# Kernel tuning notes

Measured on AMD Instinct MI355X. Metric: run time of the kernel, lower is better.

## Reference

```python
import jax, jax.numpy as jnp
import numpy as np

PAIRS = [(0,1),(1,2),(2,3),(0,4),(4,5),(5,6),(0,7),(7,8),(8,9),(9,10),(8,11),(11,12),(12,13),(8,14),(14,15),(15,16)]
END_JOINTS = np.array([3, 6, 10, 13, 16])  # leaf joints gated in the trailing loop
N, DIM, HID, B = 17, 512, 384, 8192
LN_EPS = 1e-5


def _build_adj():
    A = np.zeros((N, N), np.float32)
    for p, c in PAIRS:
        A[p, c] = A[c, p] = 1.0
    A += np.eye(N, dtype=np.float32)
    dinv = 1.0 / np.sqrt(A.sum(1))
    return jnp.asarray(dinv[:, None] * A * dinv[None, :])


def setup_inputs() -> dict:
    key = jax.random.key(0)
    ks = jax.random.split(key, 8)
    return {
        "x_gcn": jax.random.normal(ks[0], (B, N, DIM), jnp.float32),
        "bone_features": jax.random.normal(ks[1], (B, N, 192), jnp.float32),
        "adj": _build_adj(),
        "g1": jnp.ones((DIM,), jnp.float32),
        "b1": jnp.zeros((DIM,), jnp.float32),
        "W1": jax.random.normal(ks[2], (2, DIM, HID), jnp.float32) * 0.02,
        "M1": jax.random.uniform(ks[3], (N, HID), jnp.float32),
        "A2_1": jnp.ones((N, N), jnp.float32),
        "bias1": jnp.zeros((HID,), jnp.float32),
        "W2": jax.random.normal(ks[4], (2, HID, DIM), jnp.float32) * 0.02,
        "M2": jax.random.uniform(ks[5], (N, DIM), jnp.float32),
        "A2_2": jnp.ones((N, N), jnp.float32),
        "bias2": jnp.zeros((DIM,), jnp.float32),
        "g2": jnp.ones((DIM,), jnp.float32),
        "b2": jnp.zeros((DIM,), jnp.float32),
    }


def _ln(x, g, b):
    m = x.mean(-1, keepdims=True)
    v = jnp.mean((x - m) ** 2, axis=-1, keepdims=True)
    return (x - m) * jax.lax.rsqrt(v + LN_EPS) * g + b


def _mgc(x, W, M, adj_base, A2, bias):
    # Modulated graph conv: separate self / neighbor transforms, per-node modulation M.
    h0 = jnp.einsum('bnc,cd->bnd', x, W[0])
    h1 = jnp.einsum('bnc,cd->bnd', x, W[1])
    adj = adj_base + A2
    adj = (adj.T + adj) * 0.5
    E = jnp.eye(N, dtype=x.dtype)
    out = jnp.einsum('vw,bwd->bvd', adj * E, M * h0) + jnp.einsum('vw,bwd->bvd', adj * (1.0 - E), M * h1)
    return out + bias


def reference(x_gcn, bone_features, adj, g1, b1, W1, M1, A2_1, bias1,
              W2, M2, A2_2, bias2, g2, b2):
    h = _ln(x_gcn, g1, b1)
    h = _mgc(h, W1, M1, adj, A2_1, bias1)
    h = jax.nn.gelu(h, approximate=False)  # torch nn.GELU default = exact erf
    h = _mgc(h, W2, M2, adj, A2_2, bias2)
    h = _ln(h, g2, b2)
    xp = x_gcn + h  # drop_path=0 -> identity

    # bone gating: first chunk(3, -1) slice, mean over channels, sigmoid gate
    c = bone_features.shape[-1]
    bone_chunk = bone_features[..., : -(-c // 3)]  # torch.chunk first piece (ceil)
    gate = jax.nn.sigmoid(bone_chunk.mean(-1, keepdims=True) * 0.01)  # (B, N, 1)
    mask = jnp.zeros((N,), xp.dtype).at[jnp.asarray(END_JOINTS)].set(1.0)
    return xp * (1.0 + 0.03 * gate * mask[None, :, None])
```

## Files before the change

### kernel.cpp

```cpp
#include <hip/hip_runtime.h>
#include <hip/hip_bf16.h>

typedef __attribute__((ext_vector_type(8))) short s16x8;
typedef __attribute__((ext_vector_type(4))) float f32x4;

typedef __attribute__((address_space(1))) void v_as1;
typedef __attribute__((address_space(3))) void v_as3;

__device__ __forceinline__ void gload16(const void* g, void* l) {
    __builtin_amdgcn_global_load_lds((const v_as1*)g, (v_as3*)l, 16, 0, 0);
}

__device__ __forceinline__ unsigned short f2bf(float f) {
    unsigned u = __float_as_uint(f);
    unsigned r = (u + 0x7FFFu + ((u >> 16) & 1u)) >> 16;
    return (unsigned short)r;
}
__device__ __forceinline__ float frombf(unsigned short u) {
    return __uint_as_float(((unsigned)u) << 16);
}

__global__ void prep_w1(const float* __restrict__ W1, unsigned short* __restrict__ w1t) {
    int idx = blockIdx.x * 256 + threadIdx.x;
    if (idx >= 768 * 512) return;
    int n = idx >> 9, k = idx & 511;
    int g = (n >= 384) ? 1 : 0;
    int d = n - g * 384;
    w1t[idx] = f2bf(W1[((long)g * 512 + k) * 384 + d]);
}

__global__ void prep_w2(const float* __restrict__ W2, unsigned short* __restrict__ w2t) {
    int idx = blockIdx.x * 256 + threadIdx.x;
    if (idx >= 1024 * 384) return;
    int n = idx / 384, k = idx % 384;
    int g = (n >= 512) ? 1 : 0;
    int d = n - g * 512;
    w2t[idx] = f2bf(W2[((long)g * 384 + k) * 512 + d]);
}

__global__ void prep_adj(const float* __restrict__ adj, const float* __restrict__ A2a,
                         const float* __restrict__ A2b, float* __restrict__ coef1,
                         float* __restrict__ coef2) {
    int t = threadIdx.x;
    if (t < 289) {
        int v = t / 17, w = t % 17;
        int tt = w * 17 + v;
        float s1 = 0.5f * (adj[t] + A2a[t] + adj[tt] + A2a[tt]);
        float s2 = 0.5f * (adj[t] + A2b[t] + adj[tt] + A2b[tt]);
        coef1[t] = (v == w) ? 0.f : s1;
        coef2[t] = (v == w) ? 0.f : s2;
        if (v == w) { coef1[289 + v] = s1; coef2[289 + v] = s2; }
    }
}

__global__ __launch_bounds__(256) void ln1_kernel(const float* __restrict__ x,
                                                  const float* __restrict__ g,
                                                  const float* __restrict__ b,
                                                  unsigned short* __restrict__ y, int rows) {
    int wave = threadIdx.x >> 6, lane = threadIdx.x & 63;
    long row = (long)blockIdx.x * 4 + wave;
    if (row >= rows) return;
    const float4* xr = (const float4*)(x + row * 512);
    float4 v0 = xr[lane];
    float4 v1 = xr[lane + 64];
    float s = v0.x + v0.y + v0.z + v0.w + v1.x + v1.y + v1.z + v1.w;
    float q = v0.x * v0.x + v0.y * v0.y + v0.z * v0.z + v0.w * v0.w +
              v1.x * v1.x + v1.y * v1.y + v1.z * v1.z + v1.w * v1.w;
    #pragma unroll
    for (int off = 32; off; off >>= 1) { s += __shfl_xor(s, off); q += __shfl_xor(q, off); }
    float mean = s * (1.f / 512.f);
    float var  = q * (1.f / 512.f) - mean * mean;
    float rstd = rsqrtf(var + 1e-5f);
    const float4* gr = (const float4*)g;
    const float4* br = (const float4*)b;
    ushort4* yr = (ushort4*)(y + row * 512);
    #pragma unroll
    for (int i = 0; i < 2; ++i) {
        float4 vv = i ? v1 : v0;
        float4 gg = gr[lane + 64 * i];
        float4 bb = br[lane + 64 * i];
        ushort4 o;
        o.x = f2bf((vv.x - mean) * rstd * gg.x + bb.x);
        o.y = f2bf((vv.y - mean) * rstd * gg.y + bb.y);
        o.z = f2bf((vv.z - mean) * rstd * gg.z + bb.z);
        o.w = f2bf((vv.w - mean) * rstd * gg.w + bb.w);
        yr[lane + 64 * i] = o;
    }
}

__global__ __launch_bounds__(256) void gemm_bt_kernel(const unsigned short* __restrict__ A,
                                                      const unsigned short* __restrict__ Bt,
                                                      unsigned short* __restrict__ C,
                                                      int K, int Ncols, int NBX) {
    __shared__ __align__(16) unsigned short As[128 * 64];
    __shared__ __align__(16) unsigned short Bs[128 * 64];
    const int t = threadIdx.x;
    const int lane = t & 63;
    const int w = t >> 6;
    const int wr = w >> 1, wc = w & 1;

    const int nwg = gridDim.x;
    const int q = nwg >> 3, r = nwg & 7;
    const int xcd = blockIdx.x & 7, pos = blockIdx.x >> 3;
    const int wgid = (xcd < r ? xcd * (q + 1) : r * (q + 1) + (xcd - r) * q) + pos;
    const int bx = wgid % NBX;
    const int by = wgid / NBX;
    const long row0 = (long)by * 128;
    const long col0 = (long)bx * 128;

    const int lm = lane & 15;
    const int g4 = lane >> 4;
    const int swz0 = ((g4 ^ (lm & 7)) * 8);
    const int swz1 = (((g4 + 4) ^ (lm & 7)) * 8);

    f32x4 acc[4][4];
    #pragma unroll
    for (int m = 0; m < 4; ++m)
        #pragma unroll
        for (int n = 0; n < 4; ++n) acc[m][n] = (f32x4)0.f;

    const int srow = t >> 3;
    const int sslot = (t & 7) ^ (srow & 7);
    const unsigned short* aBase = A + (row0 + srow) * K + sslot * 8;
    const unsigned short* bBase = Bt + (col0 + srow) * K + sslot * 8;
    unsigned short* aDst = &As[w * 512];
    unsigned short* bDst = &Bs[w * 512];

    const int ktiles = K >> 6;
    for (int kt = 0; kt < ktiles; ++kt) {
        const long ko = (long)kt * 64;
        __syncthreads();
        #pragma unroll
        for (int rr = 0; rr < 4; ++rr) {
            gload16(aBase + (long)(rr * 32) * K + ko, aDst + rr * 2048);
            gload16(bBase + (long)(rr * 32) * K + ko, bDst + rr * 2048);
        }
        __syncthreads();
        #pragma unroll
        for (int kk = 0; kk < 2; ++kk) {
            const int so = kk ? swz1 : swz0;
            s16x8 af[4], bfv[4];
            #pragma unroll
            for (int m = 0; m < 4; ++m)
                af[m] = *(const s16x8*)&As[(wr * 64 + m * 16 + lm) * 64 + so];
            #pragma unroll
            for (int n = 0; n < 4; ++n)
                bfv[n] = *(const s16x8*)&Bs[(wc * 64 + n * 16 + lm) * 64 + so];
            #pragma unroll
            for (int m = 0; m < 4; ++m)
                #pragma unroll
                for (int n = 0; n < 4; ++n)
                    acc[m][n] = __builtin_amdgcn_mfma_f32_16x16x32_bf16(af[m], bfv[n], acc[m][n], 0, 0, 0);
        }
    }
    const int r4 = (lane >> 4) * 4;
    #pragma unroll
    for (int m = 0; m < 4; ++m) {
        #pragma unroll
        for (int j = 0; j < 4; ++j) {
            long grow = row0 + wr * 64 + m * 16 + r4 + j;
            unsigned short* crow = C + grow * Ncols + col0 + wc * 64 + lm;
            #pragma unroll
            for (int n = 0; n < 4; ++n) crow[n * 16] = f2bf(acc[m][n][j]);
        }
    }
}

__global__ __launch_bounds__(384) void mixgelu_kernel(const unsigned short* __restrict__ h,
                                                      const float* __restrict__ M1,
                                                      const float* __restrict__ coef,
                                                      const float* __restrict__ bias,
                                                      unsigned short* __restrict__ z) {
    const int t = threadIdx.x;
    const int half = t / 192;
    const int tt = t - half * 192;
    const int d0 = tt * 2;
    const long b = blockIdx.x * 2 + half;
    const unsigned short* hb = h + b * 17 * 768;

    float ax[17], ay[17];
    const float bx = bias[d0], by = bias[d0 + 1];
    #pragma unroll
    for (int v = 0; v < 17; ++v) {
        float dg = coef[289 + v];
        float2 m = *(const float2*)(M1 + v * 384 + d0);
        ushort2 hv = *(const ushort2*)(hb + v * 768 + d0);
        ax[v] = dg * m.x * frombf(hv.x) + bx;
        ay[v] = dg * m.y * frombf(hv.y) + by;
    }
    #pragma unroll
    for (int w = 0; w < 17; ++w) {
        float2 m = *(const float2*)(M1 + w * 384 + d0);
        ushort2 hw = *(const ushort2*)(hb + w * 768 + 384 + d0);
        float px = m.x * frombf(hw.x);
        float py = m.y * frombf(hw.y);
        #pragma unroll
        for (int v = 0; v < 17; ++v) {
            float c = coef[v * 17 + w];
            ax[v] += c * px;
            ay[v] += c * py;
        }
    }
    unsigned short* zb = z + b * 17 * 384 + d0;
    #pragma unroll
    for (int v = 0; v < 17; ++v) {
        float gx = 0.5f * ax[v] * (1.f + erff(ax[v] * 0.70710678118f));
        float gy = 0.5f * ay[v] * (1.f + erff(ay[v] * 0.70710678118f));
        ushort2 o; o.x = f2bf(gx); o.y = f2bf(gy);
        *(ushort2*)(zb + v * 384) = o;
    }
}

__global__ __launch_bounds__(256) void final_kernel(const unsigned short* __restrict__ h2,
                                                    const float* __restrict__ x,
                                                    const float* __restrict__ bone,
                                                    const float* __restrict__ M2,
                                                    const float* __restrict__ coef,
                                                    const float* __restrict__ bias2,
                                                    const float* __restrict__ g2,
                                                    const float* __restrict__ b2,
                                                    float* __restrict__ out) {
    __shared__ float gate[17];
    __shared__ float red[17][8];
    const int t = threadIdx.x, lane = t & 63, wave = t >> 6;
    const int d0 = t * 2;
    const long b = blockIdx.x;

    #pragma unroll
    for (int v0 = 0; v0 < 20; v0 += 4) {
        int v = v0 + wave;
        if (v < 17) {
            float s = bone[(b * 17 + v) * 192 + lane];
            #pragma unroll
            for (int off = 32; off; off >>= 1) s += __shfl_xor(s, off);
            if (lane == 0) gate[v] = 1.f / (1.f + expf(-s * (0.01f / 64.f)));
        }
    }

    const unsigned short* hb = h2 + b * 17 * 1024;
    float ax[17], ay[17];
    const float bx = bias2[d0], by = bias2[d0 + 1];
    #pragma unroll
    for (int v = 0; v < 17; ++v) {
        float dg = coef[289 + v];
        float2 m = *(const float2*)(M2 + v * 512 + d0);
        ushort2 hv = *(const ushort2*)(hb + v * 1024 + d0);
        ax[v] = dg * m.x * frombf(hv.x) + bx;
        ay[v] = dg * m.y * frombf(hv.y) + by;
    }
    #pragma unroll
    for (int w = 0; w < 17; ++w) {
        float2 m = *(const float2*)(M2 + w * 512 + d0);
        ushort2 hw = *(const ushort2*)(hb + w * 1024 + 512 + d0);
        float px = m.x * frombf(hw.x);
        float py = m.y * frombf(hw.y);
        #pragma unroll
        for (int v = 0; v < 17; ++v) {
            float c = coef[v * 17 + w];
            ax[v] += c * px;
            ay[v] += c * py;
        }
    }
    #pragma unroll
    for (int v = 0; v < 17; ++v) {
        float s = ax[v] + ay[v];
        float q = ax[v] * ax[v] + ay[v] * ay[v];
        #pragma unroll
        for (int off = 32; off; off >>= 1) { s += __shfl_xor(s, off); q += __shfl_xor(q, off); }
        if (lane == 0) { red[v][wave] = s; red[v][4 + wave] = q; }
    }
    __syncthreads();
    const float2 gg = *(const float2*)(g2 + d0);
    const float2 bb = *(const float2*)(b2 + d0);
    const float* xb = x + b * 17 * 512 + d0;
    float* ob = out + b * 17 * 512 + d0;
    #pragma unroll
    for (int v = 0; v < 17; ++v) {
        float s = red[v][0] + red[v][1] + red[v][2] + red[v][3];
        float q = red[v][4] + red[v][5] + red[v][6] + red[v][7];
        float mean = s * (1.f / 512.f);
        float rstd = rsqrtf(q * (1.f / 512.f) - mean * mean + 1e-5f);
        const bool endj = (v == 3 || v == 6 || v == 10 || v == 13 || v == 16);
        float scale = endj ? (1.f + 0.03f * gate[v]) : 1.f;
        float2 xv = *(const float2*)(xb + v * 512);
        float ox = (xv.x + (ax[v] - mean) * rstd * gg.x + bb.x) * scale;
        float oy = (xv.y + (ay[v] - mean) * rstd * gg.y + bb.y) * scale;
        *(float2*)(ob + v * 512) = make_float2(ox, oy);
    }
}

extern "C" void kernel_launch(void* const* d_in, const int* in_sizes, int n_in,
                              void* d_out, int out_size, void* d_ws, size_t ws_size,
                              hipStream_t stream) {
    const float* x     = (const float*)d_in[0];
    const float* bone  = (const float*)d_in[1];
    const float* adj   = (const float*)d_in[2];
    const float* g1    = (const float*)d_in[3];
    const float* b1    = (const float*)d_in[4];
    const float* W1    = (const float*)d_in[5];
    const float* M1    = (const float*)d_in[6];
    const float* A21   = (const float*)d_in[7];
    const float* bias1 = (const float*)d_in[8];
    const float* W2    = (const float*)d_in[9];
    const float* M2    = (const float*)d_in[10];
    const float* A22   = (const float*)d_in[11];
    const float* bias2 = (const float*)d_in[12];
    const float* g2    = (const float*)d_in[13];
    const float* b2    = (const float*)d_in[14];
    float* out = (float*)d_out;

    char* ws = (char*)d_ws;
    size_t off = 0;
    auto alloc = [&](size_t bytes) -> char* {
        char* p = ws + off;
        off = (off + bytes + 255) & ~(size_t)255;
        return p;
    };
    unsigned short* w1t = (unsigned short*)alloc(768 * 512 * 2);
    unsigned short* w2t = (unsigned short*)alloc(1024 * 384 * 2);
    float* coef1 = (float*)alloc(306 * 4);
    float* coef2 = (float*)alloc(306 * 4);
    size_t fixed = off;

    int nc = 32;
    const int cands[6] = {1, 2, 4, 8, 16, 32};
    for (int ci = 0; ci < 6; ++ci) {
        size_t Bc = 8192 / cands[ci];
        size_t need = fixed + Bc * 17 * (512 + 768 + 384 + 1024) * 2 + 4 * 256;
        if (need <= ws_size) { nc = cands[ci]; break; }
    }
    long Bc = 8192 / nc;
    unsigned short* y  = (unsigned short*)alloc(Bc * 17 * 512 * 2);
    unsigned short* h  = (unsigned short*)alloc(Bc * 17 * 768 * 2);
    unsigned short* z  = (unsigned short*)alloc(Bc * 17 * 384 * 2);
    unsigned short* h2 = (unsigned short*)alloc(Bc * 17 * 1024 * 2);

    prep_w1<<<(768 * 512 + 255) / 256, 256, 0, stream>>>(W1, w1t);
    prep_w2<<<(1024 * 384 + 255) / 256, 256, 0, stream>>>(W2, w2t);
    prep_adj<<<1, 320, 0, stream>>>(adj, A21, A22, coef1, coef2);

    int rows = (int)(Bc * 17);
    int nby = rows / 128;
    for (int c = 0; c < nc; ++c) {
        long rb = (long)c * rows;
        ln1_kernel<<<rows / 4, 256, 0, stream>>>(x + rb * 512, g1, b1, y, rows);
        gemm_bt_kernel<<<6 * nby, 256, 0, stream>>>(y, w1t, h, 512, 768, 6);
        mixgelu_kernel<<<Bc / 2, 384, 0, stream>>>(h, M1, coef1, bias1, z);
        gemm_bt_kernel<<<8 * nby, 256, 0, stream>>>(z, w2t, h2, 384, 1024, 8);
        final_kernel<<<Bc, 256, 0, stream>>>(h2, x + rb * 512, bone + rb * 192, M2, coef2,
                                             bias2, g2, b2, out + rb * 512);
    }
}
```

Baseline: 771.8 us.

## Vectorize graph-mix kernels to 4 channels per thread, stage coefficients in LDS, fast GELU

The node-mixing GELU kernel and the final LN kernel now handle four channels per thread with float4/ushort4 loads, and each block covers more batch items (4 and 2 respectively). The adjacency coefficients are transposed and staged in shared memory rather than read from global memory inside the inner loop. Exact erff is replaced by an Abramowitz-Stegun polynomial erf using rcp and exp2. The intent is fewer, wider memory transactions and less transcendental cost, at the price of more registers per thread (17 float4 accumulators) and a small approximation error in GELU.

```diff
diff --git a/kernel.cpp b/kernel.cpp
--- a/kernel.cpp
+++ b/kernel.cpp
@@ -18,6 +18,17 @@
 }
 __device__ __forceinline__ float frombf(unsigned short u) {
     return __uint_as_float(((unsigned)u) << 16);
+}
+
+__device__ __forceinline__ float gelu_fast(float v) {
+    float ax = fabsf(v) * 0.70710678118f;
+    float t = __builtin_amdgcn_rcpf(fmaf(0.3275911f, ax, 1.f));
+    float poly = t * fmaf(t, fmaf(t, fmaf(t, fmaf(t, 1.061405429f, -1.453152027f),
+                                          1.421413741f), -0.284496736f), 0.254829592f);
+    float e = exp2f(ax * ax * -1.44269504089f);
+    float er = fmaf(-poly, e, 1.f);
+    er = copysignf(er, v);
+    return 0.5f * v * (1.f + er);
 }
 
 __global__ void prep_w1(const float* __restrict__ W1, unsigned short* __restrict__ w1t) {
@@ -47,8 +58,8 @@
         int tt = w * 17 + v;
         float s1 = 0.5f * (adj[t] + A2a[t] + adj[tt] + A2a[tt]);
         float s2 = 0.5f * (adj[t] + A2b[t] + adj[tt] + A2b[tt]);
-        coef1[t] = (v == w) ? 0.f : s1;
-        coef2[t] = (v == w) ? 0.f : s2;
+        coef1[w * 17 + v] = (v == w) ? 0.f : s1;
+        coef2[w * 17 + v] = (v == w) ? 0.f : s2;
         if (v == w) { coef1[289 + v] = s1; coef2[289 + v] = s2; }
     }
 }
@@ -171,43 +182,56 @@
                                                       const float* __restrict__ coef,
                                                       const float* __restrict__ bias,
                                                       unsigned short* __restrict__ z) {
+    __shared__ float CsT[289];
+    __shared__ float Dgs[17];
     const int t = threadIdx.x;
-    const int half = t / 192;
-    const int tt = t - half * 192;
-    const int d0 = tt * 2;
-    const long b = blockIdx.x * 2 + half;
+    if (t < 289) CsT[t] = coef[t];
+    if (t >= 289 && t < 306) Dgs[t - 289] = coef[t];
+    __syncthreads();
+    const int bi_ = t / 96;
+    const int tt = t - bi_ * 96;
+    const int d0 = tt * 4;
+    const long b = (long)blockIdx.x * 4 + bi_;
     const unsigned short* hb = h + b * 17 * 768;
-
-    float ax[17], ay[17];
-    const float bx = bias[d0], by = bias[d0 + 1];
-    #pragma unroll
-    for (int v = 0; v < 17; ++v) {
-        float dg = coef[289 + v];
-        float2 m = *(const float2*)(M1 + v * 384 + d0);
-        ushort2 hv = *(const ushort2*)(hb + v * 768 + d0);
-        ax[v] = dg * m.x * frombf(hv.x) + bx;
-        ay[v] = dg * m.y * frombf(hv.y) + by;
+    const float4 bv = *(const float4*)(bias + d0);
+    float4 a[17];
+    #pragma unroll
+    for (int v = 0; v < 17; ++v) {
+        float dg = Dgs[v];
+        float4 m = *(const float4*)(M1 + v * 384 + d0);
+        ushort4 hv = *(const ushort4*)(hb + v * 768 + d0);
+        a[v].x = dg * m.x * frombf(hv.x) + bv.x;
+        a[v].y = dg * m.y * frombf(hv.y) + bv.y;
+        a[v].z = dg * m.z * frombf(hv.z) + bv.z;
+        a[v].w = dg * m.w * frombf(hv.w) + bv.w;
     }
     #pragma unroll
     for (int w = 0; w < 17; ++w) {
-        float2 m = *(const float2*)(M1 + w * 384 + d0);
-        ushort2 hw = *(const ushort2*)(hb + w * 768 + 384 + d0);
-        float px = m.x * frombf(hw.x);
-        float py = m.y * frombf(hw.y);
+        float4 m = *(const float4*)(M1 + w * 384 + d0);
+        ushort4 hw = *(const ushort4*)(hb + w * 768 + 384 + d0);
+        float4 p;
+        p.x = m.x * frombf(hw.x);
+        p.y = m.y * frombf(hw.y);
+        p.z = m.z * frombf(hw.z);
+        p.w = m.w * frombf(hw.w);
         #pragma unroll
         for (int v = 0; v < 17; ++v) {
-            float c = coef[v * 17 + w];
-            ax[v] += c * px;
-            ay[v] += c * py;
+            float c = CsT[w * 17 + v];
+            a[v].x += c * p.x;
+            a[v].y += c * p.y;
+            a[v].z += c * p.z;
+            a[v].w += c * p.w;
         }
     }
     unsigned short* zb = z + b * 17 * 384 + d0;
     #pragma unroll
     for (int v = 0; v < 17; ++v) {
-        float gx = 0.5f * ax[v] * (1.f + erff(ax[v] * 0.70710678118f));
-        float gy = 0.5f * ay[v] * (1.f + erff(ay[v] * 0.70710678118f));
-        ushort2 o; o.x = f2bf(gx); o.y = f2bf(gy);
-        *(ushort2*)(zb + v * 384) = o;
+        ushort4 o;
+        o.x = f2bf(gelu_fast(a[v].x));
+        o.y = f2bf(gelu_fast(a[v].y));
+        o.z = f2bf(gelu_fast(a[v].z));
+        o.w = f2bf(gelu_fast(a[v].w));
+        *(ushort4*)(zb + v * 384) = o;
     }
 }
 
@@ -220,72 +244,86 @@
                                                     const float* __restrict__ g2,
                                                     const float* __restrict__ b2,
                                                     float* __restrict__ out) {
-    __shared__ float gate[17];
-    __shared__ float red[17][8];
+    __shared__ float CsT[289];
+    __shared__ float Dgs[17];
+    __shared__ float gate[2][17];
+    __shared__ float red[2][17][4];
     const int t = threadIdx.x, lane = t & 63, wave = t >> 6;
-    const int d0 = t * 2;
-    const long b = blockIdx.x;
-
-    #pragma unroll
-    for (int v0 = 0; v0 < 20; v0 += 4) {
-        int v = v0 + wave;
-        if (v < 17) {
-            float s = bone[(b * 17 + v) * 192 + lane];
-            #pragma unroll
-            for (int off = 32; off; off >>= 1) s += __shfl_xor(s, off);
-            if (lane == 0) gate[v] = 1.f / (1.f + expf(-s * (0.01f / 64.f)));
-        }
-    }
-
-    const unsigned short* hb = h2 + b * 17 * 1024;
-    float ax[17], ay[17];
-    const float bx = bias2[d0], by = bias2[d0 + 1];
-    #pragma unroll
-    for (int v = 0; v < 17; ++v) {
-        float dg = coef[289 + v];
-        float2 m = *(const float2*)(M2 + v * 512 + d0);
-        ushort2 hv = *(const ushort2*)(hb + v * 1024 + d0);
-        ax[v] = dg * m.x * frombf(hv.x) + bx;
-        ay[v] = dg * m.y * frombf(hv.y) + by;
+    for (int i = t; i < 289; i += 256) CsT[i] = coef[i];
+    if (t < 17) Dgs[t] = coef[289 + t];
+    const int hb_ = wave >> 1;
+    const int wh = wave & 1;
+    const long b = (long)blockIdx.x * 2 + hb_;
+    __syncthreads();
+
+    for (int v = wh; v < 17; v += 2) {
+        float s = bone[(b * 17 + v) * 192 + lane];
+        #pragma unroll
+        for (int off = 32; off; off >>= 1) s += __shfl_xor(s, off);
+        if (lane == 0) gate[hb_][v] = 1.f / (1.f + expf(-s * (0.01f / 64.f)));
+    }
+
+    const int tt = t & 127;
+    const int d0 = tt * 4;
+    const unsigned short* hbp = h2 + b * 17 * 1024;
+    const float4 bv = *(const float4*)(bias2 + d0);
+    float4 a[17];
+    #pragma unroll
+    for (int v = 0; v < 17; ++v) {
+        float dg = Dgs[v];
+        float4 m = *(const float4*)(M2 + v * 512 + d0);
+        ushort4 hv = *(const ushort4*)(hbp + v * 1024 + d0);
+        a[v].x = dg * m.x * frombf(hv.x) + bv.x;
+        a[v].y = dg * m.y * frombf(hv.y) + bv.y;
+        a[v].z = dg * m.z * frombf(hv.z) + bv.z;
+        a[v].w = dg * m.w * frombf(hv.w) + bv.w;
     }
     #pragma unroll
     for (int w = 0; w < 17; ++w) {
-        float2 m = *(const float2*)(M2 + w * 512 + d0);
-        ushort2 hw = *(const ushort2*)(hb + w * 1024 + 512 + d0);
-        float px = m.x * frombf(hw.x);
-        float py = m.y * frombf(hw.y);
+        float4 m = *(const float4*)(M2 + w * 512 + d0);
+        ushort4 hw = *(const ushort4*)(hbp + w * 1024 + 512 + d0);
+        float4 p;
+        p.x = m.x * frombf(hw.x);
+        p.y = m.y * frombf(hw.y);
+        p.z = m.z * frombf(hw.z);
+        p.w = m.w * frombf(hw.w);
         #pragma unroll
         for (int v = 0; v < 17; ++v) {
-            float c = coef[v * 17 + w];
-            ax[v] += c * px;
-            ay[v] += c * py;
-        }
-    }
-    #pragma unroll
-    for (int v = 0; v < 17; ++v) {
-        float s = ax[v] + ay[v];
-        float q = ax[v] * ax[v] + ay[v] * ay[v];
+            float c = CsT[w * 17 + v];
+            a[v].x += c * p.x;
+            a[v].y += c * p.y;
+            a[v].z += c * p.z;
+            a[v].w += c * p.w;
+        }
+    }
+    #pragma unroll
+    for (int v = 0; v < 17; ++v) {
+        float s = (a[v].x + a[v].y) + (a[v].z + a[v].w);
+        float q = a[v].x * a[v].x + a[v].y * a[v].y + a[v].z * a[v].z + a[v].w * a[v].w;
         #pragma unroll
         for (int off = 32; off; off >>= 1) { s += __shfl_xor(s, off); q += __shfl_xor(q, off); }
-        if (lane == 0) { red[v][wave] = s; red[v][4 + wave] = q; }
+        if (lane == 0) { red[hb_][v][wh] = s; red[hb_][v][2 + wh] = q; }
     }
     __syncthreads();
-    const float2 gg = *(const float2*)(g2 + d0);
-    const float2 bb = *(const float2*)(b2 + d0);
+    const float4 gg = *(const float4*)(g2 + d0);
+    const float4 bb = *(const float4*)(b2 + d0);
     const float* xb = x + b * 17 * 512 + d0;
     float* ob = out + b * 17 * 512 + d0;
     #pragma unroll
     for (int v = 0; v < 17; ++v) {
-        float s = red[v][0] + red[v][1] + red[v][2] + red[v][3];
-        float q = red[v][4] + red[v][5] + red[v][6] + red[v][7];
+        float s = red[hb_][v][0] + red[hb_][v][1];
+        float q = red[hb_][v][2] + red[hb_][v][3];
         float mean = s * (1.f / 512.f);
         float rstd = rsqrtf(q * (1.f / 512.f) - mean * mean + 1e-5f);
         const bool endj = (v == 3 || v == 6 || v == 10 || v == 13 || v == 16);
-        float scale = endj ? (1.f + 0.03f * gate[v]) : 1.f;
-        float2 xv = *(const float2*)(xb + v * 512);
-        float ox = (xv.x + (ax[v] - mean) * rstd * gg.x + bb.x) * scale;
-        float oy = (xv.y + (ay[v] - mean) * rstd * gg.y + bb.y) * scale;
-        *(float2*)(ob + v * 512) = make_float2(ox, oy);
+        float scale = endj ? (1.f + 0.03f * gate[hb_][v]) : 1.f;
+        float4 xv = *(const float4*)(xb + v * 512);
+        float4 o;
+        o.x = (xv.x + (a[v].x - mean) * rstd * gg.x + bb.x) * scale;
+        o.y = (xv.y + (a[v].y - mean) * rstd * gg.y + bb.y) * scale;
+        o.z = (xv.z + (a[v].z - mean) * rstd * gg.z + bb.z) * scale;
+        o.w = (xv.w + (a[v].w - mean) * rstd * gg.w + bb.w) * scale;
+        *(float4*)(ob + v * 512) = o;
     }
 }
 
@@ -345,9 +383,9 @@
         long rb = (long)c * rows;
         ln1_kernel<<<rows / 4, 256, 0, stream>>>(x + rb * 512, g1, b1, y, rows);
         gemm_bt_kernel<<<6 * nby, 256, 0, stream>>>(y, w1t, h, 512, 768, 6);
-        mixgelu_kernel<<<Bc / 2, 384, 0, stream>>>(h, M1, coef1, bias1, z);
+        mixgelu_kernel<<<Bc / 4, 384, 0, stream>>>(h, M1, coef1, bias1, z);
         gemm_bt_kernel<<<8 * nby, 256, 0, stream>>>(z, w2t, h2, 384, 1024, 8);
-        final_kernel<<<Bc, 256, 0, stream>>>(h2, x + rb * 512, bone + rb * 192, M2, coef2,
-                                             bias2, g2, b2, out + rb * 512);
-    }
-}
+        final_kernel<<<Bc / 2, 256, 0, stream>>>(h2, x + rb * 512, bone + rb * 192, M2, coef2,
+                                                 bias2, g2, b2, out + rb * 512);
+    }
+}
```

After: 983.4 us. +27.4%, slower.
